# Kernel optimization log

Hardware: AMD Instinct MI355X
Metric: run time of the kernel (lower is better)

Reference implementation:

```python
import jax, jax.numpy as jnp
import numpy as np


def setup_inputs() -> dict:
    key = jax.random.key(0)
    kx, kk, kq, kv = jax.random.split(key, 4)
    B, T, C = 4, 2048, 1024
    scale = 1.0 / np.sqrt(C)
    x = jax.random.normal(kx, (B, T, C), dtype=jnp.float32)
    # nn.Linear(C, C, bias=False): y = x @ W.T, W is [C, C]
    Wk = jax.random.normal(kk, (C, C), dtype=jnp.float32) * scale
    Wq = jax.random.normal(kq, (C, C), dtype=jnp.float32) * scale
    Wv = jax.random.normal(kv, (C, C), dtype=jnp.float32) * scale
    return {"x": x, "Wk": Wk, "Wq": Wq, "Wv": Wv}


def reference(x, Wk, Wq, Wv):
    B, T, C = x.shape
    k = jnp.einsum('btc,dc->btd', x, Wk)  # [B,T,C]
    q = jnp.einsum('btc,dc->btd', x, Wq)
    v = jnp.einsum('btc,dc->btd', x, Wv)
    # full T x T score matrix, scaled by C**-0.5 (note: C, not head_dim split)
    wei = jnp.einsum('btd,bsd->bts', q, k) * (C ** -0.5)  # [B,T,T]
    causal = jnp.tril(jnp.ones((T, T), dtype=bool))
    wei = jnp.where(causal, wei, -jnp.inf)
    wei = jax.nn.softmax(wei, axis=-1)
    # dropout(p=0.1) omitted: reference is eval-mode (identity)
    out = jnp.einsum('bts,bsd->btd', wei, v)  # [B,T,C]
    return out
```

## Files before the change

### kernel.cpp

```cpp
#include <hip/hip_runtime.h>
#include <cstdio>
#include <cmath>

#define TSEQ 2048
#define CDIM 1024
#define NBATCH 4

typedef float f32x4 __attribute__((ext_vector_type(4)));
typedef __bf16 bf16x8 __attribute__((ext_vector_type(8)));
typedef unsigned short u16;

__device__ __forceinline__ u16 f2bf(float f) {
  unsigned u = __builtin_bit_cast(unsigned, f);
  unsigned r = (u + 0x7FFFu + ((u >> 16) & 1u)) >> 16;
  return (u16)r;
}

__device__ __forceinline__ void gload_lds16(const void* g, void* l) {
  __builtin_amdgcn_global_load_lds(
      (__attribute__((address_space(1))) void*)g,
      (__attribute__((address_space(3))) void*)l, 16, 0, 0);
}

#define SWZ2(b_) ((b_) ^ ((((b_) >> 7) & 7) << 4))

__device__ __forceinline__ void gemm128(
    const u16* __restrict__ A, const u16* __restrict__ B,
    int lda, int ldb, int m0, int n0, int nT,
    char* smem, f32x4 acc[4][4])
{
  u16* Ab = (u16*)smem;
  u16* Bb = (u16*)(smem + 32768);
  const int tid = threadIdx.x, w = tid >> 6, l = tid & 63;
  const int wr = w >> 1, wc = w & 1;
  const int frow = l & 15, fko = l >> 4;
  const int srow = l >> 3;
  const int scol = ((l & 7) * 8) ^ (((l >> 3) & 7) << 3);

  const u16* gA = A + (size_t)(m0 + w * 32 + srow) * lda + scol;
  const u16* gB = B + (size_t)(n0 + w * 32 + srow) * ldb + scol;

  auto stageA = [&](int t) {
    if (t >= nT) return;
    const u16* s = gA + t * 64;
    u16* d = Ab + (t & 1) * 8192 + w * 2048;
    gload_lds16(s, d);
    gload_lds16(s + (size_t)8 * lda, d + 512);
    gload_lds16(s + (size_t)16 * lda, d + 1024);
    gload_lds16(s + (size_t)24 * lda, d + 1536);
  };
  auto stageB = [&](int t) {
    if (t >= nT) return;
    const u16* s = gB + t * 64;
    u16* d = Bb + (t & 1) * 8192 + w * 2048;
    gload_lds16(s, d);
    gload_lds16(s + (size_t)8 * ldb, d + 512);
    gload_lds16(s + (size_t)16 * ldb, d + 1024);
    gload_lds16(s + (size_t)24 * ldb, d + 1536);
  };

#define AOFF(mf, ks) SWZ2(((wr * 64 + (mf) * 16 + frow) * 128 + (ks) * 64 + fko * 16))
#define BOFF(nf, ks) SWZ2(((wc * 64 + (nf) * 16 + frow) * 128 + (ks) * 64 + fko * 16))

  stageB(0); stageA(0); stageB(1); stageA(1);
  asm volatile("s_waitcnt vmcnt(8)" ::: "memory");
  __builtin_amdgcn_s_barrier();

#pragma unroll 1
  for (int t = 0; t < nT; ++t) {
    const char* Abase = (const char*)Ab + (t & 1) * 16384;
    const char* Bbase = (const char*)Bb + (t & 1) * 16384;
    bf16x8 bfr[4][2], af0[2][2];
#pragma unroll
    for (int nf = 0; nf < 4; ++nf)
#pragma unroll
      for (int ks = 0; ks < 2; ++ks)
        bfr[nf][ks] = *(const bf16x8*)(Bbase + BOFF(nf, ks));
#pragma unroll
    for (int mm = 0; mm < 2; ++mm)
#pragma unroll
      for (int ks = 0; ks < 2; ++ks)
        af0[mm][ks] = *(const bf16x8*)(Abase + AOFF(mm, ks));
    __builtin_amdgcn_sched_barrier(0);
    stageB(t + 2);
    __builtin_amdgcn_s_barrier();
    __builtin_amdgcn_s_setprio(1);
#pragma unroll
    for (int ks = 0; ks < 2; ++ks)
#pragma unroll
      for (int mm = 0; mm < 2; ++mm)
#pragma unroll
        for (int nf = 0; nf < 4; ++nf)
          acc[mm][nf] = __builtin_amdgcn_mfma_f32_16x16x32_bf16(
              af0[mm][ks], bfr[nf][ks], acc[mm][nf], 0, 0, 0);
    __builtin_amdgcn_s_setprio(0);
    __builtin_amdgcn_s_barrier();
    bf16x8 af1[2][2];
#pragma unroll
    for (int mm = 0; mm < 2; ++mm)
#pragma unroll
      for (int ks = 0; ks < 2; ++ks)
        af1[mm][ks] = *(const bf16x8*)(Abase + AOFF(2 + mm, ks));
    __builtin_amdgcn_sched_barrier(0);
    stageA(t + 2);
    __builtin_amdgcn_s_barrier();
    __builtin_amdgcn_s_setprio(1);
#pragma unroll
    for (int ks = 0; ks < 2; ++ks)
#pragma unroll
      for (int mm = 0; mm < 2; ++mm)
#pragma unroll
        for (int nf = 0; nf < 4; ++nf)
          acc[2 + mm][nf] = __builtin_amdgcn_mfma_f32_16x16x32_bf16(
              af1[mm][ks], bfr[nf][ks], acc[2 + mm][nf], 0, 0, 0);
    __builtin_amdgcn_s_setprio(0);
    if (t < nT - 2) asm volatile("s_waitcnt vmcnt(8)" ::: "memory");
    else if (t == nT - 2) asm volatile("s_waitcnt vmcnt(0)" ::: "memory");
    __builtin_amdgcn_s_barrier();
  }
#undef AOFF
#undef BOFF
}

#define ACC_ZERO4(acc)                                  \
  _Pragma("unroll") for (int m_ = 0; m_ < 4; ++m_)      \
  _Pragma("unroll") for (int n_ = 0; n_ < 4; ++n_)      \
      acc[m_][n_] = (f32x4){0.f, 0.f, 0.f, 0.f};

__global__ void __launch_bounds__(256) k_cvt_all(
    const float* __restrict__ x, const float* __restrict__ Wk,
    const float* __restrict__ Wq, const float* __restrict__ Wv,
    u16* __restrict__ xb, u16* __restrict__ wb)
{
  const int NX4 = (NBATCH * TSEQ * CDIM) / 4;
  const int NW4 = (CDIM * CDIM) / 4;
  int g = blockIdx.x * 256 + threadIdx.x;
  const float* src; u16* dst; int i;
  if (g < NX4) { src = x; dst = xb; i = g; }
  else {
    int g2 = g - NX4;
    int w = g2 / NW4; i = g2 - w * NW4;
    src = (w == 0) ? Wk : (w == 1) ? Wq : Wv;
    dst = wb + (size_t)w * CDIM * CDIM;
  }
  float4 v = ((const float4*)src)[i];
  ushort4 o;
  o.x = f2bf(v.x); o.y = f2bf(v.y); o.z = f2bf(v.z); o.w = f2bf(v.w);
  ((ushort4*)dst)[i] = o;
}

__global__ void __launch_bounds__(256, 2) k_gemm_qkv_t(
    const u16* __restrict__ xb, const u16* __restrict__ wb,
    u16* __restrict__ kb, u16* __restrict__ qb, u16* __restrict__ vb)
{
  extern __shared__ char smem[];
  const int id = blockIdx.x;
  const int xcd = id & 7, loc = id >> 3;
  const int mt = xcd * 8 + (loc & 7);
  const int nt = loc >> 3;
  const int m0 = mt * 128, n0g = nt * 128;

  f32x4 acc[4][4];
  ACC_ZERO4(acc);
  gemm128(xb, wb, CDIM, CDIM, m0, n0g, 16, smem, acc);

  const int tid = threadIdx.x, w = tid >> 6, l = tid & 63;
  const int wr = w >> 1, wc = w & 1;
  const int frow = l & 15, fko = l >> 4;
  const int z = n0g >> 10;
  u16* outp = (z == 0) ? kb : (z == 1) ? qb : vb;
  const float scale = (z == 1) ? 0.03125f : 1.0f;
  const int r0 = m0 + wr * 64 + fko * 4;
  const int c0 = (n0g & 1023) + wc * 64 + frow;
#pragma unroll
  for (int mf = 0; mf < 4; ++mf)
#pragma unroll
    for (int nf = 0; nf < 4; ++nf) {
      const int r = r0 + mf * 16;
      const int c = c0 + nf * 16;
#pragma unroll
      for (int j = 0; j < 4; ++j)
        outp[(size_t)(r + j) * CDIM + c] = f2bf(acc[mf][nf][j] * scale);
    }
}

__global__ void __launch_bounds__(256, 2) k_gemm_scores_t(
    const u16* __restrict__ qb, const u16* __restrict__ kb,
    u16* __restrict__ pb, float* __restrict__ rs)
{
  extern __shared__ char smem[];
  const int id = blockIdx.x;
  const int sw = (id & 7) * 68 + (id >> 3);
  const int b = sw / 136;
  const int wq = sw - b * 136;
  int y = (int)((sqrtf(8.f * wq + 1.f) - 1.f) * 0.5f);
  while ((y + 1) * (y + 2) / 2 <= wq) ++y;
  while (y * (y + 1) / 2 > wq) --y;
  const int xt = wq - y * (y + 1) / 2;
  const int m0 = y * 128, n0 = xt * 128;

  const u16* A = qb + (size_t)b * TSEQ * CDIM;
  const u16* B = kb + (size_t)b * TSEQ * CDIM;
  u16* P = pb + (size_t)b * TSEQ * TSEQ;

  f32x4 acc[4][4];
  ACC_ZERO4(acc);
  gemm128(A, B, CDIM, CDIM, m0, n0, 16, smem, acc);

  const int tid = threadIdx.x, w = tid >> 6, l = tid & 63;
  const int wr = w >> 1, wc = w & 1;
  const int frow = l & 15, fko = l >> 4;
  float* rowpart = (float*)smem;

#pragma unroll
  for (int mf = 0; mf < 4; ++mf) {
#pragma unroll
    for (int j = 0; j < 4; ++j) {
      const int rloc = wr * 64 + mf * 16 + fko * 4 + j;
      const int rglob = m0 + rloc;
      float p4 = 0.f;
#pragma unroll
      for (int nf = 0; nf < 4; ++nf) {
        const int c = n0 + wc * 64 + nf * 16 + frow;
        float e = (c <= rglob) ? __expf(acc[mf][nf][j]) : 0.f;
        p4 += e;
        P[(size_t)rglob * TSEQ + c] = f2bf(e);
      }
#pragma unroll
      for (int d = 1; d < 16; d <<= 1) p4 += __shfl_xor(p4, d);
      if (frow == 0) rowpart[rloc * 2 + wc] = p4;
    }
  }
  __syncthreads();
  if (tid < 128)
    rs[((size_t)b * 16 + xt) * TSEQ + m0 + tid] =
        rowpart[tid * 2] + rowpart[tid * 2 + 1];
}

__global__ void __launch_bounds__(256) k_transpose_v(const u16* __restrict__ vb,
                                                     u16* __restrict__ vt) {
  __shared__ u16 tile[32][33];
  const int b = blockIdx.z;
  const u16* V = vb + (size_t)b * TSEQ * CDIM;
  u16* Vt = vt + (size_t)b * CDIM * TSEQ;
  const int c0 = blockIdx.x * 32, r0 = blockIdx.y * 32;
  const int tx = threadIdx.x, ty = threadIdx.y;
#pragma unroll
  for (int j = 0; j < 4; ++j)
    tile[ty + j * 8][tx] = V[(size_t)(r0 + ty + j * 8) * CDIM + c0 + tx];
  __syncthreads();
#pragma unroll
  for (int j = 0; j < 4; ++j)
    Vt[(size_t)(c0 + ty + j * 8) * TSEQ + r0 + tx] = tile[tx][ty + j * 8];
}

__global__ void __launch_bounds__(256) k_suminv(const float* __restrict__ rs,
                                                float* __restrict__ inv) {
  const int i = blockIdx.x * 256 + threadIdx.x;
  const int b = i >> 11, t = i & (TSEQ - 1), y = t >> 7;
  const float* p = rs + (size_t)b * 16 * TSEQ + t;
  float s = 0.f;
  for (int x = 0; x <= y; ++x) s += p[(size_t)x * TSEQ];
  inv[i] = 1.f / s;
}

__global__ void __launch_bounds__(256, 2) k_gemm_pv_t(
    const u16* __restrict__ pb, const u16* __restrict__ vt,
    const float* __restrict__ inv, float* __restrict__ out)
{
  extern __shared__ char smem[];
  const int id = blockIdx.x;
  const int n = id & 7, loc = id >> 3;
  const int b = loc >> 4, mt = loc & 15;
  const int m0 = mt * 128, n0 = n * 128;
  const int nT = 2 * (mt + 1);

  const u16* A = pb + (size_t)b * TSEQ * TSEQ;
  const u16* B = vt + (size_t)b * CDIM * TSEQ;
  float* O = out + (size_t)b * TSEQ * CDIM;

  f32x4 acc[4][4];
  ACC_ZERO4(acc);
  gemm128(A, B, TSEQ, TSEQ, m0, n0, nT, smem, acc);

  const int tid = threadIdx.x, w = tid >> 6, l = tid & 63;
  const int wr = w >> 1, wc = w & 1;
  const int frow = l & 15, fko = l >> 4;
#pragma unroll
  for (int mf = 0; mf < 4; ++mf) {
    const int r = m0 + wr * 64 + mf * 16 + fko * 4;
    const float4 iv = *(const float4*)&inv[(size_t)b * TSEQ + r];
    const float ivj[4] = {iv.x, iv.y, iv.z, iv.w};
#pragma unroll
    for (int nf = 0; nf < 4; ++nf) {
      const int c = n0 + wc * 64 + nf * 16 + frow;
#pragma unroll
      for (int j = 0; j < 4; ++j)
        O[(size_t)(r + j) * CDIM + c] = acc[mf][nf][j] * ivj[j];
    }
  }
}

extern "C" void kernel_launch(void* const* d_in, const int* in_sizes, int n_in,
                              void* d_out, int out_size, void* d_ws, size_t ws_size,
                              hipStream_t stream) {
  const float* x  = (const float*)d_in[0];
  const float* Wk = (const float*)d_in[1];
  const float* Wq = (const float*)d_in[2];
  const float* Wv = (const float*)d_in[3];
  float* out = (float*)d_out;

  const size_t M = (size_t)NBATCH * TSEQ;

  size_t off = 0;
  auto alloc = [&](size_t bytes) {
    void* p = (char*)d_ws + off;
    off += (bytes + 255) & ~(size_t)255;
    return p;
  };
  u16* xb = (u16*)alloc(M * CDIM * 2);
  u16* wb = (u16*)alloc(3ull * CDIM * CDIM * 2);
  u16* qb = (u16*)alloc(M * CDIM * 2);
  u16* kb = (u16*)alloc(M * CDIM * 2);
  u16* vb = (u16*)alloc(M * CDIM * 2);
  u16* pbuf = (u16*)alloc((size_t)NBATCH * TSEQ * TSEQ * 2);
  float* rs  = (float*)alloc((size_t)NBATCH * 16 * TSEQ * 4);
  float* inv = (float*)alloc(M * 4);
  if (off > ws_size) {
    fprintf(stderr, "kernel_launch: ws too small: need %zu, have %zu\n", off, ws_size);
    return;
  }
  u16* vt = xb;

  const int NX4 = (NBATCH * TSEQ * CDIM) / 4;
  const int NW4 = (CDIM * CDIM) / 4;
  const int cvtBlocks = (NX4 + 3 * NW4) / 256;

  static_cast<void>(hipFuncSetAttribute(
      reinterpret_cast<const void*>(k_gemm_qkv_t),
      hipFuncAttributeMaxDynamicSharedMemorySize, 65536));
  static_cast<void>(hipFuncSetAttribute(
      reinterpret_cast<const void*>(k_gemm_scores_t),
      hipFuncAttributeMaxDynamicSharedMemorySize, 65536));
  static_cast<void>(hipFuncSetAttribute(
      reinterpret_cast<const void*>(k_gemm_pv_t),
      hipFuncAttributeMaxDynamicSharedMemorySize, 65536));

  k_cvt_all<<<cvtBlocks, 256, 0, stream>>>(x, Wk, Wq, Wv, xb, wb);
  k_gemm_qkv_t<<<1536, 256, 65536, stream>>>(xb, wb, kb, qb, vb);
  k_transpose_v<<<dim3(CDIM / 32, TSEQ / 32, NBATCH), dim3(32, 8), 0, stream>>>(vb, vt);
  k_gemm_scores_t<<<544, 256, 65536, stream>>>(qb, kb, pbuf, rs);
  k_suminv<<<(int)(M / 256), 256, 0, stream>>>(rs, inv);
  k_gemm_pv_t<<<512, 256, 65536, stream>>>(pbuf, vt, inv, out);
}
```

Measured before the change: 150.8 us.

## Use 128x256 tiles with split-phase pipelined K-loop for QKV projection GEMM

Replaces the 128x128 tile GEMM in the QKV projection with a new 128x256 tile routine that uses a K step of 32, double-buffered LDS staging, and interleaves B-half loads with MFMA phases under setprio. This halves the grid to 768 blocks and reduces LDS to 48KB. The aim is more reuse of the A tile per load and better overlap of global-to-LDS traffic with compute. In exchange, each thread holds twice as many accumulators, which raises register pressure, and there are fewer blocks to spread across CUs.

```diff
diff --git a/kernel.cpp b/kernel.cpp
--- a/kernel.cpp
+++ b/kernel.cpp
@@ -20,6 +20,93 @@
   __builtin_amdgcn_global_load_lds(
       (__attribute__((address_space(1))) void*)g,
       (__attribute__((address_space(3))) void*)l, 16, 0, 0);
+}
+
+__device__ __forceinline__ void gemm128x256(
+    const u16* __restrict__ A, const u16* __restrict__ B,
+    int lda, int ldb, int m0, int n0, int nT,
+    char* smem, f32x4 acc[4][8])
+{
+  u16* Ab = (u16*)smem;
+  u16* Bb = (u16*)(smem + 16384);
+  const int tid = threadIdx.x, w = tid >> 6, l = tid & 63;
+  const int wr = w >> 1, wcB = w & 1;
+  const int frow = l & 15, fko = l >> 4;
+  const int swzr = (l & 3) ^ ((l >> 2) & 3);
+  const int srow = l >> 2;
+  const int sg = ((l & 3) ^ ((l >> 2) & 3) ^ ((l >> 4) & 3)) * 8;
+
+  const u16* gA = A + (size_t)(m0 + w * 32 + srow) * lda + sg;
+  const u16* gB = B + (size_t)(n0 + w * 64 + srow) * ldb + sg;
+
+  auto stageA = [&](int t) {
+    if (t >= nT) return;
+    const u16* s = gA + t * 32;
+    u16* d = Ab + (t & 1) * 4096 + w * 1024;
+    gload_lds16(s, d);
+    gload_lds16(s + (size_t)16 * lda, d + 512);
+  };
+  auto stageB = [&](int t) {
+    if (t >= nT) return;
+    const u16* s = gB + t * 32;
+    u16* d = Bb + (t & 1) * 8192 + w * 2048;
+    gload_lds16(s, d);
+    gload_lds16(s + (size_t)16 * ldb, d + 512);
+    gload_lds16(s + (size_t)32 * ldb, d + 1024);
+    gload_lds16(s + (size_t)48 * ldb, d + 1536);
+  };
+
+#define AOFF(mf) (((wr * 64 + (mf) * 16 + frow) * 64) + ((fko ^ swzr) * 16))
+#define BOFF(nf) (((wcB * 128 + (nf) * 16 + frow) * 64) + ((fko ^ swzr) * 16))
+
+  stageA(0); stageB(0); stageA(1); stageB(1);
+  asm volatile("s_waitcnt vmcnt(6)" ::: "memory");
+  __builtin_amdgcn_s_barrier();
+
+#pragma unroll 1
+  for (int t = 0; t < nT; ++t) {
+    const char* Abase = (const char*)Ab + (t & 1) * 8192;
+    const char* Bbase = (const char*)Bb + (t & 1) * 16384;
+    bf16x8 af[4], bf0[4];
+#pragma unroll
+    for (int mf = 0; mf < 4; ++mf)
+      af[mf] = *(const bf16x8*)(Abase + AOFF(mf));
+#pragma unroll
+    for (int nf = 0; nf < 4; ++nf)
+      bf0[nf] = *(const bf16x8*)(Bbase + BOFF(nf));
+    __builtin_amdgcn_sched_barrier(0);
+    stageA(t + 2);
+    __builtin_amdgcn_s_barrier();
+    __builtin_amdgcn_s_setprio(1);
+#pragma unroll
+    for (int mf = 0; mf < 4; ++mf)
+#pragma unroll
+      for (int nf = 0; nf < 4; ++nf)
+        acc[mf][nf] = __builtin_amdgcn_mfma_f32_16x16x32_bf16(
+            af[mf], bf0[nf], acc[mf][nf], 0, 0, 0);
+    __builtin_amdgcn_s_setprio(0);
+    __builtin_amdgcn_s_barrier();
+    bf16x8 bf1[4];
+#pragma unroll
+    for (int nf = 0; nf < 4; ++nf)
+      bf1[nf] = *(const bf16x8*)(Bbase + BOFF(4 + nf));
+    __builtin_amdgcn_sched_barrier(0);
+    stageB(t + 2);
+    __builtin_amdgcn_s_barrier();
+    __builtin_amdgcn_s_setprio(1);
+#pragma unroll
+    for (int mf = 0; mf < 4; ++mf)
+#pragma unroll
+      for (int nf = 0; nf < 4; ++nf)
+        acc[mf][4 + nf] = __builtin_amdgcn_mfma_f32_16x16x32_bf16(
+            af[mf], bf1[nf], acc[mf][4 + nf], 0, 0, 0);
+    __builtin_amdgcn_s_setprio(0);
+    if (t < nT - 2) asm volatile("s_waitcnt vmcnt(6)" ::: "memory");
+    else if (t == nT - 2) asm volatile("s_waitcnt vmcnt(0)" ::: "memory");
+    __builtin_amdgcn_s_barrier();
+  }
+#undef AOFF
+#undef BOFF
 }
 
 #define SWZ2(b_) ((b_) ^ ((((b_) >> 7) & 7) << 4))
@@ -158,24 +245,28 @@
   const int xcd = id & 7, loc = id >> 3;
   const int mt = xcd * 8 + (loc & 7);
   const int nt = loc >> 3;
-  const int m0 = mt * 128, n0g = nt * 128;
-
-  f32x4 acc[4][4];
-  ACC_ZERO4(acc);
-  gemm128(xb, wb, CDIM, CDIM, m0, n0g, 16, smem, acc);
+  const int m0 = mt * 128, n0g = nt * 256;
+
+  f32x4 acc[4][8];
+#pragma unroll
+  for (int m_ = 0; m_ < 4; ++m_)
+#pragma unroll
+    for (int n_ = 0; n_ < 8; ++n_) acc[m_][n_] = (f32x4){0.f, 0.f, 0.f, 0.f};
+
+  gemm128x256(xb, wb, CDIM, CDIM, m0, n0g, 32, smem, acc);
 
   const int tid = threadIdx.x, w = tid >> 6, l = tid & 63;
-  const int wr = w >> 1, wc = w & 1;
+  const int wr = w >> 1, wcB = w & 1;
   const int frow = l & 15, fko = l >> 4;
   const int z = n0g >> 10;
   u16* outp = (z == 0) ? kb : (z == 1) ? qb : vb;
   const float scale = (z == 1) ? 0.03125f : 1.0f;
   const int r0 = m0 + wr * 64 + fko * 4;
-  const int c0 = (n0g & 1023) + wc * 64 + frow;
+  const int c0 = (n0g & 1023) + wcB * 128 + frow;
 #pragma unroll
   for (int mf = 0; mf < 4; ++mf)
 #pragma unroll
-    for (int nf = 0; nf < 4; ++nf) {
+    for (int nf = 0; nf < 8; ++nf) {
       const int r = r0 + mf * 16;
       const int c = c0 + nf * 16;
 #pragma unroll
@@ -338,7 +429,7 @@
 
   static_cast<void>(hipFuncSetAttribute(
       reinterpret_cast<const void*>(k_gemm_qkv_t),
-      hipFuncAttributeMaxDynamicSharedMemorySize, 65536));
+      hipFuncAttributeMaxDynamicSharedMemorySize, 49152));
   static_cast<void>(hipFuncSetAttribute(
       reinterpret_cast<const void*>(k_gemm_scores_t),
       hipFuncAttributeMaxDynamicSharedMemorySize, 65536));
@@ -347,7 +438,7 @@
       hipFuncAttributeMaxDynamicSharedMemorySize, 65536));
 
   k_cvt_all<<<cvtBlocks, 256, 0, stream>>>(x, Wk, Wq, Wv, xb, wb);
-  k_gemm_qkv_t<<<1536, 256, 65536, stream>>>(xb, wb, kb, qb, vb);
+  k_gemm_qkv_t<<<768, 256, 49152, stream>>>(xb, wb, kb, qb, vb);
   k_transpose_v<<<dim3(CDIM / 32, TSEQ / 32, NBATCH), dim3(32, 8), 0, stream>>>(vb, vt);
   k_gemm_scores_t<<<544, 256, 65536, stream>>>(qb, kb, pbuf, rs);
   k_suminv<<<(int)(M / 256), 256, 0, stream>>>(rs, inv);
```

Measured after the change: 152.4 us. No clear change (+1.1%).

## Fuse V transpose into QKV GEMM epilogue and row-sum inverse into PV GEMM

Applied to the files above, without the earlier changes.

The QKV GEMM epilogue for V tiles now stages the tile transposed in shared memory and writes V^T directly with 16-byte stores, which removes the separate transpose kernel and its extra pass over V. The PV GEMM now reduces the per-tile row-sum partials and takes their reciprocal in shared memory before scaling, which removes the suminv kernel and the inv buffer. Together this cuts two launches and some global traffic. In exchange, V tiles pay an extra LDS round trip and the PV epilogue adds a small serial reduction.

```diff
diff --git a/kernel.cpp b/kernel.cpp
--- a/kernel.cpp
+++ b/kernel.cpp
@@ -151,7 +151,7 @@
 
 __global__ void __launch_bounds__(256, 2) k_gemm_qkv_t(
     const u16* __restrict__ xb, const u16* __restrict__ wb,
-    u16* __restrict__ kb, u16* __restrict__ qb, u16* __restrict__ vb)
+    u16* __restrict__ kb, u16* __restrict__ qb, u16* __restrict__ vt)
 {
   extern __shared__ char smem[];
   const int id = blockIdx.x;
@@ -168,20 +168,46 @@
   const int wr = w >> 1, wc = w & 1;
   const int frow = l & 15, fko = l >> 4;
   const int z = n0g >> 10;
-  u16* outp = (z == 0) ? kb : (z == 1) ? qb : vb;
-  const float scale = (z == 1) ? 0.03125f : 1.0f;
-  const int r0 = m0 + wr * 64 + fko * 4;
-  const int c0 = (n0g & 1023) + wc * 64 + frow;
-#pragma unroll
-  for (int mf = 0; mf < 4; ++mf)
-#pragma unroll
-    for (int nf = 0; nf < 4; ++nf) {
-      const int r = r0 + mf * 16;
-      const int c = c0 + nf * 16;
-#pragma unroll
-      for (int j = 0; j < 4; ++j)
-        outp[(size_t)(r + j) * CDIM + c] = f2bf(acc[mf][nf][j] * scale);
+  if (z < 2) {
+    u16* outp = (z == 0) ? kb : qb;
+    const float scale = (z == 1) ? 0.03125f : 1.0f;
+    const int r0 = m0 + wr * 64 + fko * 4;
+    const int c0 = (n0g & 1023) + wc * 64 + frow;
+#pragma unroll
+    for (int mf = 0; mf < 4; ++mf)
+#pragma unroll
+      for (int nf = 0; nf < 4; ++nf) {
+        const int r = r0 + mf * 16;
+        const int c = c0 + nf * 16;
+#pragma unroll
+        for (int j = 0; j < 4; ++j)
+          outp[(size_t)(r + j) * CDIM + c] = f2bf(acc[mf][nf][j] * scale);
+      }
+  } else {
+    __syncthreads();
+    u16* tile = (u16*)smem;
+#pragma unroll
+    for (int mf = 0; mf < 4; ++mf)
+#pragma unroll
+      for (int nf = 0; nf < 4; ++nf) {
+        const int cl = wc * 64 + nf * 16 + frow;
+        const int rl = wr * 64 + mf * 16 + fko * 4;
+#pragma unroll
+        for (int j = 0; j < 4; ++j)
+          tile[cl * 136 + rl + j] = f2bf(acc[mf][nf][j]);
+      }
+    __syncthreads();
+    const int b = m0 >> 11, t0 = m0 & 2047;
+    const int c0g = n0g - 2048;
+    u16* dst = vt + ((size_t)b * CDIM + c0g) * TSEQ + t0;
+#pragma unroll
+    for (int it = 0; it < 8; ++it) {
+      const int idx = it * 256 + tid;
+      const int c = idx >> 4, ch = idx & 15;
+      bf16x8 v = *(const bf16x8*)(tile + c * 136 + ch * 8);
+      *(bf16x8*)(dst + (size_t)c * TSEQ + ch * 8) = v;
     }
+  }
 }
 
 __global__ void __launch_bounds__(256, 2) k_gemm_scores_t(
@@ -237,36 +263,9 @@
         rowpart[tid * 2] + rowpart[tid * 2 + 1];
 }
 
-__global__ void __launch_bounds__(256) k_transpose_v(const u16* __restrict__ vb,
-                                                     u16* __restrict__ vt) {
-  __shared__ u16 tile[32][33];
-  const int b = blockIdx.z;
-  const u16* V = vb + (size_t)b * TSEQ * CDIM;
-  u16* Vt = vt + (size_t)b * CDIM * TSEQ;
-  const int c0 = blockIdx.x * 32, r0 = blockIdx.y * 32;
-  const int tx = threadIdx.x, ty = threadIdx.y;
-#pragma unroll
-  for (int j = 0; j < 4; ++j)
-    tile[ty + j * 8][tx] = V[(size_t)(r0 + ty + j * 8) * CDIM + c0 + tx];
-  __syncthreads();
-#pragma unroll
-  for (int j = 0; j < 4; ++j)
-    Vt[(size_t)(c0 + ty + j * 8) * TSEQ + r0 + tx] = tile[tx][ty + j * 8];
-}
-
-__global__ void __launch_bounds__(256) k_suminv(const float* __restrict__ rs,
-                                                float* __restrict__ inv) {
-  const int i = blockIdx.x * 256 + threadIdx.x;
-  const int b = i >> 11, t = i & (TSEQ - 1), y = t >> 7;
-  const float* p = rs + (size_t)b * 16 * TSEQ + t;
-  float s = 0.f;
-  for (int x = 0; x <= y; ++x) s += p[(size_t)x * TSEQ];
-  inv[i] = 1.f / s;
-}
-
 __global__ void __launch_bounds__(256, 2) k_gemm_pv_t(
     const u16* __restrict__ pb, const u16* __restrict__ vt,
-    const float* __restrict__ inv, float* __restrict__ out)
+    const float* __restrict__ rs, float* __restrict__ out)
 {
   extern __shared__ char smem[];
   const int id = blockIdx.x;
@@ -286,10 +285,22 @@
   const int tid = threadIdx.x, w = tid >> 6, l = tid & 63;
   const int wr = w >> 1, wc = w & 1;
   const int frow = l & 15, fko = l >> 4;
+
+  __syncthreads();
+  float* sinv = (float*)smem;
+  if (tid < 128) {
+    float s = 0.f;
+    const float* p = rs + (size_t)b * 16 * TSEQ + m0 + tid;
+    for (int x = 0; x <= mt; ++x) s += p[(size_t)x * TSEQ];
+    sinv[tid] = 1.f / s;
+  }
+  __syncthreads();
+
 #pragma unroll
   for (int mf = 0; mf < 4; ++mf) {
-    const int r = m0 + wr * 64 + mf * 16 + fko * 4;
-    const float4 iv = *(const float4*)&inv[(size_t)b * TSEQ + r];
+    const int rloc = wr * 64 + mf * 16 + fko * 4;
+    const int r = m0 + rloc;
+    const float4 iv = *(const float4*)&sinv[rloc];
     const float ivj[4] = {iv.x, iv.y, iv.z, iv.w};
 #pragma unroll
     for (int nf = 0; nf < 4; ++nf) {
@@ -322,15 +333,13 @@
   u16* wb = (u16*)alloc(3ull * CDIM * CDIM * 2);
   u16* qb = (u16*)alloc(M * CDIM * 2);
   u16* kb = (u16*)alloc(M * CDIM * 2);
-  u16* vb = (u16*)alloc(M * CDIM * 2);
+  u16* vt = (u16*)alloc(M * CDIM * 2);
   u16* pbuf = (u16*)alloc((size_t)NBATCH * TSEQ * TSEQ * 2);
-  float* rs  = (float*)alloc((size_t)NBATCH * 16 * TSEQ * 4);
-  float* inv = (float*)alloc(M * 4);
+  float* rs = (float*)alloc((size_t)NBATCH * 16 * TSEQ * 4);
   if (off > ws_size) {
     fprintf(stderr, "kernel_launch: ws too small: need %zu, have %zu\n", off, ws_size);
     return;
   }
-  u16* vt = xb;
 
   const int NX4 = (NBATCH * TSEQ * CDIM) / 4;
   const int NW4 = (CDIM * CDIM) / 4;
@@ -347,9 +356,7 @@
       hipFuncAttributeMaxDynamicSharedMemorySize, 65536));
 
   k_cvt_all<<<cvtBlocks, 256, 0, stream>>>(x, Wk, Wq, Wv, xb, wb);
-  k_gemm_qkv_t<<<1536, 256, 65536, stream>>>(xb, wb, kb, qb, vb);
-  k_transpose_v<<<dim3(CDIM / 32, TSEQ / 32, NBATCH), dim3(32, 8), 0, stream>>>(vb, vt);
+  k_gemm_qkv_t<<<1536, 256, 65536, stream>>>(xb, wb, kb, qb, vt);
   k_gemm_scores_t<<<544, 256, 65536, stream>>>(qb, kb, pbuf, rs);
-  k_suminv<<<(int)(M / 256), 256, 0, stream>>>(rs, inv);
-  k_gemm_pv_t<<<512, 256, 65536, stream>>>(pbuf, vt, inv, out);
-}
+  k_gemm_pv_t<<<512, 256, 65536, stream>>>(pbuf, vt, rs, out);
+}
```

Result: faster. 139.5 us (-7.5%).
